# Optimization experiments

Measured on AMD Instinct MI355X. Metric: run time of the kernel, lower is better.

The kernel has to match this reference:

```python
import jax, jax.numpy as jnp
import numpy as np

K = 16  # neighbors per node (dgl.knn_graph k)


def _knn_indices(centers, k):
    # pairwise squared distances [N, N]
    sq = jnp.sum(centers * centers, axis=1)
    d2 = sq[:, None] + sq[None, :] - 2.0 * (centers @ centers.T)
    # k nearest (includes self at distance ~0), edges: neighbor(src) -> node(dst)
    _, idx = jax.lax.top_k(-d2, k)  # [N, k]
    return idx


def _graph_conv(h, idx, src_norm, dst_norm, W, b):
    # DGL GraphConv, norm='both': D_out^{-1/2} A D_in^{-1/2} H W + b
    hs = h * src_norm[:, None]          # scale by out-degree^{-1/2}
    agg = jnp.sum(hs[idx], axis=1)      # sum over k neighbors -> [N, F]
    agg = agg * dst_norm                # in-degree is exactly k for knn graph
    return agg @ W + b


def setup_inputs() -> dict:
    key = jax.random.key(0)
    ks = jax.random.split(key, 8)
    N, D, H = 20000, 128, 256
    s_in, s_h = 1.0 / np.sqrt(D), 1.0 / np.sqrt(H)
    return {
        "x": jax.random.normal(ks[0], (N, D), dtype=jnp.float32),
        "centers": jax.random.normal(ks[1], (N, 3), dtype=jnp.float32),
        "W0": jax.random.normal(ks[2], (D, H), dtype=jnp.float32) * s_in,
        "b0": jnp.zeros((H,), dtype=jnp.float32),
        "W1": jax.random.normal(ks[3], (H, H), dtype=jnp.float32) * s_h,
        "b1": jnp.zeros((H,), dtype=jnp.float32),
        "W2": jax.random.normal(ks[4], (H, H), dtype=jnp.float32) * s_h,
        "b2": jnp.zeros((H,), dtype=jnp.float32),
        "Wf": jax.random.normal(ks[5], (H, 1), dtype=jnp.float32) * s_h,
        "bf": jnp.zeros((1,), dtype=jnp.float32),
    }


def reference(x, centers, W0, b0, W1, b1, W2, b2, Wf, bf):
    N = x.shape[0]
    idx = _knn_indices(centers, K)  # [N, K] src nodes per dst node
    # out-degree of each node = number of times it appears as a neighbor
    out_deg = jnp.zeros((N,), dtype=x.dtype).at[idx.reshape(-1)].add(1.0)
    src_norm = jax.lax.rsqrt(jnp.maximum(out_deg, 1.0))
    dst_norm = 1.0 / jnp.sqrt(jnp.asarray(K, dtype=x.dtype))  # in-degree == K
    h = x
    for W, b in ((W0, b0), (W1, b1), (W2, b2)):
        h = jax.nn.relu(_graph_conv(h, idx, src_norm, dst_norm, W, b))
    logits = (h @ Wf + bf).squeeze(-1)  # [N]
    return jax.nn.sigmoid(logits)
```

## Files before the change

### kernel.cpp

```cpp
#include <hip/hip_runtime.h>
#include <math.h>

#define KNN 16
#define G 32
#define G3 32768
#define MRING 31
#define FLTMAX 3.402823466e+38f

typedef __attribute__((ext_vector_type(8))) short short8x;
typedef __attribute__((ext_vector_type(4))) float f32x4;

__device__ __forceinline__ unsigned short bf16rn(float x) {
  unsigned u = __float_as_uint(x);
  unsigned r = (u + 0x7FFFu + ((u >> 16) & 1u)) >> 16;
  return (unsigned short)r;
}
__device__ __forceinline__ float bf16tof(unsigned short h) {
  return __uint_as_float(((unsigned)h) << 16);
}

__device__ __forceinline__ unsigned fkey(float f) {
  unsigned u = __float_as_uint(f);
  return (u & 0x80000000u) ? ~u : (u | 0x80000000u);
}
__device__ __forceinline__ float funkey(unsigned u) {
  unsigned b = (u & 0x80000000u) ? (u & 0x7FFFFFFFu) : ~u;
  return __uint_as_float(b);
}

__device__ __forceinline__ void cell_of(float x, float y, float z, const float* P,
                                        int& cx, int& cy, int& cz) {
  cx = min(G - 1, max(0, (int)((x - P[0]) * P[3])));
  cy = min(G - 1, max(0, (int)((y - P[1]) * P[4])));
  cz = min(G - 1, max(0, (int)((z - P[2]) * P[5])));
}

__global__ void init_kernel(int* __restrict__ counts, int* __restrict__ cursor,
                            unsigned* __restrict__ bbox) {
  int t = blockIdx.x * blockDim.x + threadIdx.x;
  if (t < G3) counts[t] = 0;
  int u = t - G3;
  if (u >= 0 && u < G3) cursor[u] = 0;
  if (t == 0) {
    for (int k = 0; k < 3; ++k) { bbox[k] = 0xFFFFFFFFu; bbox[3 + k] = 0u; }
  }
}

__global__ void prep_kernel(const float* __restrict__ centers,
                            float4* __restrict__ cpack,
                            int* __restrict__ deg, unsigned* __restrict__ bbox, int n) {
  #pragma clang fp contract(off)
  int i = blockIdx.x * blockDim.x + threadIdx.x;
  if (i < n) {
    float x = centers[3 * i], y = centers[3 * i + 1], z = centers[3 * i + 2];
    float sq = (x * x + y * y) + z * z;
    cpack[i] = make_float4(x, y, z, sq);
    deg[i] = 0;
    atomicMin(&bbox[0], fkey(x));
    atomicMin(&bbox[1], fkey(y));
    atomicMin(&bbox[2], fkey(z));
    atomicMax(&bbox[3], fkey(x));
    atomicMax(&bbox[4], fkey(y));
    atomicMax(&bbox[5], fkey(z));
  }
}

__global__ void params_kernel(const unsigned* __restrict__ bbox, float* __restrict__ P) {
  if (threadIdx.x == 0 && blockIdx.x == 0) {
    float xmin = funkey(bbox[0]), ymin = funkey(bbox[1]), zmin = funkey(bbox[2]);
    float xmax = funkey(bbox[3]), ymax = funkey(bbox[4]), zmax = funkey(bbox[5]);
    float ex = fmaxf(xmax - xmin, 1e-9f);
    float ey = fmaxf(ymax - ymin, 1e-9f);
    float ez = fmaxf(zmax - zmin, 1e-9f);
    P[0] = xmin; P[1] = ymin; P[2] = zmin;
    P[3] = (float)G / ex; P[4] = (float)G / ey; P[5] = (float)G / ez;
    P[6] = ex / (float)G; P[7] = ey / (float)G; P[8] = ez / (float)G;
    P[9] = fminf(P[6], fminf(P[7], P[8]));
  }
}

__global__ void count_kernel(const float4* __restrict__ cpack, const float* __restrict__ P,
                             int* __restrict__ counts, int n) {
  int i = blockIdx.x * blockDim.x + threadIdx.x;
  if (i >= n) return;
  float4 c = cpack[i];
  int cx, cy, cz; cell_of(c.x, c.y, c.z, P, cx, cy, cz);
  atomicAdd(&counts[(cz * G + cy) * G + cx], 1);
}

__global__ __launch_bounds__(1024) void scan_kernel(const int* __restrict__ counts,
                                                    int* __restrict__ starts,
                                                    int2* __restrict__ cellinfo) {
  __shared__ int sh[1024];
  int t = threadIdx.x;
  int base = t * 32;
  int loc[32];
  int cnts[32];
  int s = 0;
  #pragma unroll
  for (int u = 0; u < 32; ++u) {
    cnts[u] = counts[base + u];
    loc[u] = s; s += cnts[u];
  }
  sh[t] = s;
  __syncthreads();
  for (int off = 1; off < 1024; off <<= 1) {
    int v = (t >= off) ? sh[t - off] : 0;
    __syncthreads();
    sh[t] += v;
    __syncthreads();
  }
  int pre = (t == 0) ? 0 : sh[t - 1];
  #pragma unroll
  for (int u = 0; u < 32; ++u) {
    int st = pre + loc[u];
    starts[base + u] = st;
    cellinfo[base + u] = make_int2(st, cnts[u]);
  }
}

__global__ void scatter_kernel(const float4* __restrict__ cpack, const float* __restrict__ P,
                               const int* __restrict__ starts, int* __restrict__ cursor,
                               int* __restrict__ sid, float4* __restrict__ spack, int n) {
  int i = blockIdx.x * blockDim.x + threadIdx.x;
  if (i >= n) return;
  float4 c = cpack[i];
  int cx, cy, cz; cell_of(c.x, c.y, c.z, P, cx, cy, cz);
  int cell = (cz * G + cy) * G + cx;
  int slot = starts[cell] + atomicAdd(&cursor[cell], 1);
  sid[slot] = i;
  spack[slot] = c;
}

__global__ __launch_bounds__(256) void query_kernel(
    const float4* __restrict__ spack, const int* __restrict__ sid,
    const int2* __restrict__ cellinfo, const float* __restrict__ P,
    int* __restrict__ knn_idx, int* __restrict__ deg, int n) {
  #pragma clang fp contract(off)
  __shared__ unsigned long long lsk[4][KNN][64];
  const int lane = threadIdx.x & 63;
  const int wv = threadIdx.x >> 6;
  const int g = blockIdx.x * 4 + wv;
  if (g >= n) return;
  const float4 q = spack[g];
  const int me = sid[g];
  const float xmin = P[0], ymin = P[1], zmin = P[2];
  const float wx = P[6], wy = P[7], wz = P[8], wmin = P[9];
  int cx, cy, cz; cell_of(q.x, q.y, q.z, P, cx, cy, cz);

  int cnt = 0;
  unsigned long long wkey = 0; int wslot = 0;
  unsigned long long minkey = ~0ull; int minslot = 0;

  for (int m = 1; m <= MRING; ++m) {
    if (m >= 2) {
      float b = (float)(m - 1) * wmin;
      float b2 = b * b * 0.999f;
      unsigned long long tk = ((unsigned long long)fkey(b2)) << 32;
      int c = 0;
      for (int t = 0; t < cnt; ++t) c += (lsk[wv][t][lane] < tk) ? 1 : 0;
      #pragma unroll
      for (int off = 1; off < 64; off <<= 1) c += __shfl_xor(c, off);
      if (c >= KNN) break;
    }
    float lw = (cnt == KNN) ? funkey((unsigned)(wkey >> 32)) : FLTMAX;
    #pragma unroll
    for (int off = 1; off < 64; off <<= 1) lw = fminf(lw, __shfl_xor(lw, off));

    const int ncells = (m == 1) ? 27 : (24 * m * m + 2);
    for (int cb = 0; cb < ncells; cb += 64) {
      int f = cb + lane;
      int ccnt = 0, cs0 = 0;
      if (f < ncells) {
        int dx, dy, dz;
        if (m == 1) {
          dz = f / 9 - 1; int rem = f % 9; dy = rem / 3 - 1; dx = rem % 3 - 1;
        } else {
          int side = 2 * m + 1;
          int S1 = side * side;
          if (f < 2 * S1) {
            dz = (f < S1) ? -m : m;
            int i2 = (f < S1) ? f : f - S1;
            dy = i2 / side - m; dx = i2 % side - m;
          } else {
            int r = f - 2 * S1;
            int layer = r / (8 * m);
            int t2 = r - layer * 8 * m;
            dz = layer - (m - 1);
            if (t2 < side) { dy = -m; dx = t2 - m; }
            else if (t2 < 2 * side) { dy = m; dx = (t2 - side) - m; }
            else { int u = t2 - 2 * side; dx = (u & 1) ? m : -m; dy = (u >> 1) - (m - 1); }
          }
        }
        int x = cx + dx, y = cy + dy, z = cz + dz;
        if (x >= 0 && x < G && y >= 0 && y < G && z >= 0 && z < G) {
          int cell = (z * G + y) * G + x;
          int2 ci = cellinfo[cell];
          if (ci.y > 0) {
            float lox = xmin + (float)x * wx;
            float loy = ymin + (float)y * wy;
            float loz = zmin + (float)z * wz;
            float ddx = fmaxf(fmaxf(lox - q.x, q.x - (lox + wx)), 0.f);
            float ddy = fmaxf(fmaxf(loy - q.y, q.y - (loy + wy)), 0.f);
            float ddz = fmaxf(fmaxf(loz - q.z, q.z - (loz + wz)), 0.f);
            float cd2 = ddx * ddx + ddy * ddy + ddz * ddz;
            if (!(cd2 * 0.999f > lw)) { ccnt = ci.y; cs0 = ci.x; }
          }
        }
      }
      int inc = ccnt;
      #pragma unroll
      for (int off = 1; off < 64; off <<= 1) {
        int t = __shfl_up(inc, off);
        if (lane >= off) inc += t;
      }
      int total = __shfl(inc, 63);
      if (total == 0) continue;
      unsigned seg = ((unsigned)(inc - ccnt) << 16) | (unsigned)cs0;
      const int tmax = total - 1;

      int fc = lane;
      int fcc = min(fc, tmax);
      int lo = 0;
      #pragma unroll
      for (int s = 32; s >= 1; s >>= 1) {
        int cand = lo + s;
        unsigned o = __shfl(seg, cand & 63);
        if (cand < 64 && (int)(o >> 16) <= fcc) lo = cand;
      }
      unsigned o2 = __shfl(seg, lo);
      int src = (int)(o2 & 0xFFFFu) + (fcc - (int)(o2 >> 16));
      float4 c4 = spack[src];
      int j = sid[src];
      const int nloop = (total + 63) >> 6;
      for (int it = 0; it < nloop; ++it) {
        int fn = fc + 64;
        int fnc = min(fn, tmax);
        int lo2 = 0;
        #pragma unroll
        for (int s = 32; s >= 1; s >>= 1) {
          int cand = lo2 + s;
          unsigned o = __shfl(seg, cand & 63);
          if (cand < 64 && (int)(o >> 16) <= fnc) lo2 = cand;
        }
        unsigned o3 = __shfl(seg, lo2);
        int srcn = (int)(o3 & 0xFFFFu) + (fnc - (int)(o3 >> 16));
        float4 c4n = spack[srcn];
        int jn = sid[srcn];
        if (fc < total) {
          float dot = fmaf(q.z, c4.z, fmaf(q.y, c4.y, q.x * c4.x));
          float d2 = (q.w + c4.w) - 2.0f * dot;
          unsigned long long key =
              (((unsigned long long)fkey(d2)) << 32) | (unsigned)j;
          if (cnt < KNN) {
            lsk[wv][cnt][lane] = key;
            if (key < minkey) { minkey = key; minslot = cnt; }
            ++cnt;
            if (cnt == KNN) {
              wkey = 0; wslot = 0;
              #pragma unroll
              for (int u = 0; u < KNN; ++u) {
                unsigned long long k2 = lsk[wv][u][lane];
                if (k2 > wkey) { wkey = k2; wslot = u; }
              }
            }
          } else if (key < wkey) {
            lsk[wv][wslot][lane] = key;
            if (key < minkey) { minkey = key; minslot = wslot; }
            wkey = 0;
            #pragma unroll
            for (int u = 0; u < KNN; ++u) {
              unsigned long long k2 = lsk[wv][u][lane];
              if (k2 > wkey) { wkey = k2; wslot = u; }
            }
          }
        }
        fc = fn; c4 = c4n; j = jn;
      }
    }
  }

  unsigned long long mykey = 0;
  for (int t = 0; t < KNN; ++t) {
    unsigned long long k = minkey; int src = lane;
    #pragma unroll
    for (int off = 1; off < 64; off <<= 1) {
      unsigned long long ok = __shfl_xor(k, off);
      int os = __shfl_xor(src, off);
      if (ok < k) { k = ok; src = os; }
    }
    if (lane == t) mykey = k;
    if (lane == src) {
      lsk[wv][minslot][lane] = ~0ull;
      minkey = ~0ull; minslot = 0;
      for (int u = 0; u < cnt; ++u) {
        unsigned long long kk = lsk[wv][u][lane];
        if (kk < minkey) { minkey = kk; minslot = u; }
      }
    }
  }
  if (lane < KNN) {
    int j = (int)(unsigned)(mykey & 0xFFFFFFFFull);
    knn_idx[me * KNN + lane] = j;
    atomicAdd(&deg[j], 1);
  }
}

__global__ void norm_kernel(const int* __restrict__ deg, float* __restrict__ srcn, int n) {
  int i = blockIdx.x * blockDim.x + threadIdx.x;
  if (i < n) {
    float d = (float)max(deg[i], 1);
    srcn[i] = 1.0f / sqrtf(d);
  }
}

__global__ void split_w_kernel(const float* __restrict__ W,
                               unsigned short* __restrict__ wbh,
                               unsigned short* __restrict__ wbl, int K) {
  int t = blockIdx.x * blockDim.x + threadIdx.x;
  int noct = (K >> 5) * 1024;
  if (t >= noct) return;
  int kblk = t >> 10;
  int g = (t >> 6) & 15;
  int l = t & 63;
  int n = ((g >> 2) << 6) + ((g & 3) << 4) + (l & 15);
  int kbase = (kblk << 5) + ((l >> 4) << 3);
  #pragma unroll
  for (int j = 0; j < 8; ++j) {
    float w = W[(kbase + j) * 256 + n];
    unsigned short hi = bf16rn(w);
    wbh[t * 8 + j] = hi;
    wbl[t * 8 + j] = bf16rn(w - bf16tof(hi));
  }
}

template <int F>
__global__ __launch_bounds__(256) void agg_kernel(const float* __restrict__ h,
                                                  const float* __restrict__ srcn,
                                                  const int* __restrict__ idx,
                                                  unsigned short* __restrict__ ah,
                                                  unsigned short* __restrict__ al,
                                                  int n) {
  const int lane = threadIdx.x & 63;
  const int wv = threadIdx.x >> 6;
  const int i = blockIdx.x * 4 + wv;
  if (i >= n) return;
  constexpr int V = F / 64;
  if constexpr (V == 4) {
    float4 acc = make_float4(0.f, 0.f, 0.f, 0.f);
    #pragma unroll
    for (int k = 0; k < KNN; ++k) {
      int s = idx[i * KNN + k];
      float sn = srcn[s];
      float4 hv = ((const float4*)(h + (size_t)s * F))[lane];
      acc.x = fmaf(sn, hv.x, acc.x);
      acc.y = fmaf(sn, hv.y, acc.y);
      acc.z = fmaf(sn, hv.z, acc.z);
      acc.w = fmaf(sn, hv.w, acc.w);
    }
    acc.x *= 0.25f; acc.y *= 0.25f; acc.z *= 0.25f; acc.w *= 0.25f;
    ushort4 hh, ll;
    hh.x = bf16rn(acc.x); ll.x = bf16rn(acc.x - bf16tof(hh.x));
    hh.y = bf16rn(acc.y); ll.y = bf16rn(acc.y - bf16tof(hh.y));
    hh.z = bf16rn(acc.z); ll.z = bf16rn(acc.z - bf16tof(hh.z));
    hh.w = bf16rn(acc.w); ll.w = bf16rn(acc.w - bf16tof(hh.w));
    ((ushort4*)(ah + (size_t)i * F))[lane] = hh;
    ((ushort4*)(al + (size_t)i * F))[lane] = ll;
  } else {
    float2 acc = make_float2(0.f, 0.f);
    #pragma unroll
    for (int k = 0; k < KNN; ++k) {
      int s = idx[i * KNN + k];
      float sn = srcn[s];
      float2 hv = ((const float2*)(h + (size_t)s * F))[lane];
      acc.x = fmaf(sn, hv.x, acc.x);
      acc.y = fmaf(sn, hv.y, acc.y);
    }
    acc.x *= 0.25f; acc.y *= 0.25f;
    ushort2 hh, ll;
    hh.x = bf16rn(acc.x); ll.x = bf16rn(acc.x - bf16tof(hh.x));
    hh.y = bf16rn(acc.y); ll.y = bf16rn(acc.y - bf16tof(hh.y));
    ((ushort2*)(ah + (size_t)i * F))[lane] = hh;
    ((ushort2*)(al + (size_t)i * F))[lane] = ll;
  }
}

__global__ __launch_bounds__(256) void gemm_mfma(
    const unsigned short* __restrict__ ah, const unsigned short* __restrict__ al,
    const unsigned short* __restrict__ wbh, const unsigned short* __restrict__ wbl,
    const float* __restrict__ bias, float* __restrict__ C, int M, int Kd) {
  __shared__ unsigned short sa_h[2][64][8];
  __shared__ unsigned short sa_l[2][64][8];
  __shared__ unsigned short sb_h[16][64][8];
  __shared__ unsigned short sb_l[16][64][8];
  const int tid = threadIdx.x;
  const int lane = tid & 63;
  const int w = tid >> 6;
  const int mt0 = blockIdx.x * 32;

  f32x4 acc[2][4];
  #pragma unroll
  for (int ms = 0; ms < 2; ++ms)
    #pragma unroll
    for (int ns = 0; ns < 4; ++ns) acc[ms][ns] = (f32x4){0.f, 0.f, 0.f, 0.f};

  const int nkb = Kd >> 5;
  for (int kit = 0; kit < nkb; ++kit) {
    const int k0 = kit << 5;
    if (tid < 128) {
      int msub = tid >> 6, l = tid & 63;
      int row = mt0 + (msub << 4) + (l & 15);
      int kk = k0 + ((l >> 4) << 3);
      if (row < M) {
        *(uint4*)&sa_h[msub][l][0] = *(const uint4*)(ah + (size_t)row * Kd + kk);
        *(uint4*)&sa_l[msub][l][0] = *(const uint4*)(al + (size_t)row * Kd + kk);
      } else {
        uint4 z = make_uint4(0, 0, 0, 0);
        *(uint4*)&sa_h[msub][l][0] = z;
        *(uint4*)&sa_l[msub][l][0] = z;
      }
    }
    #pragma unroll
    for (int o = tid; o < 1024; o += 256) {
      size_t off = ((size_t)kit * 1024 + o) * 8;
      *(uint4*)&sb_h[o >> 6][o & 63][0] = *(const uint4*)(wbh + off);
      *(uint4*)&sb_l[o >> 6][o & 63][0] = *(const uint4*)(wbl + off);
    }
    __syncthreads();
    short8x a_h0 = *(const short8x*)&sa_h[0][lane][0];
    short8x a_h1 = *(const short8x*)&sa_h[1][lane][0];
    short8x a_l0 = *(const short8x*)&sa_l[0][lane][0];
    short8x a_l1 = *(const short8x*)&sa_l[1][lane][0];
    #pragma unroll
    for (int ns = 0; ns < 4; ++ns) {
      short8x b_h = *(const short8x*)&sb_h[w * 4 + ns][lane][0];
      short8x b_l = *(const short8x*)&sb_l[w * 4 + ns][lane][0];
      acc[0][ns] = __builtin_amdgcn_mfma_f32_16x16x32_bf16(a_h0, b_h, acc[0][ns], 0, 0, 0);
      acc[0][ns] = __builtin_amdgcn_mfma_f32_16x16x32_bf16(a_h0, b_l, acc[0][ns], 0, 0, 0);
      acc[0][ns] = __builtin_amdgcn_mfma_f32_16x16x32_bf16(a_l0, b_h, acc[0][ns], 0, 0, 0);
      acc[1][ns] = __builtin_amdgcn_mfma_f32_16x16x32_bf16(a_h1, b_h, acc[1][ns], 0, 0, 0);
      acc[1][ns] = __builtin_amdgcn_mfma_f32_16x16x32_bf16(a_h1, b_l, acc[1][ns], 0, 0, 0);
      acc[1][ns] = __builtin_amdgcn_mfma_f32_16x16x32_bf16(a_l1, b_h, acc[1][ns], 0, 0, 0);
    }
    __syncthreads();
  }

  const int col = lane & 15;
  const int rq = lane >> 4;
  #pragma unroll
  for (int ms = 0; ms < 2; ++ms) {
    #pragma unroll
    for (int ns = 0; ns < 4; ++ns) {
      int nn = (w << 6) + (ns << 4) + col;
      float bi = bias[nn];
      #pragma unroll
      for (int r = 0; r < 4; ++r) {
        int row = mt0 + (ms << 4) + (rq << 2) + r;
        if (row < M) C[(size_t)row * 256 + nn] = fmaxf(acc[ms][ns][r] + bi, 0.f);
      }
    }
  }
}

__global__ __launch_bounds__(256) void final_kernel(const float* __restrict__ h,
                                                    const float* __restrict__ Wf,
                                                    const float* __restrict__ bf,
                                                    float* __restrict__ out, int n) {
  const int lane = threadIdx.x & 63;
  const int wv = threadIdx.x >> 6;
  const int i = blockIdx.x * 4 + wv;
  if (i >= n) return;
  float4 hv = *(const float4*)(h + (size_t)i * 256 + lane * 4);
  float4 wf = *(const float4*)(Wf + lane * 4);
  float p = hv.x * wf.x + hv.y * wf.y + hv.z * wf.z + hv.w * wf.w;
  #pragma unroll
  for (int off = 32; off > 0; off >>= 1) p += __shfl_down(p, off);
  if (lane == 0) out[i] = 1.0f / (1.0f + expf(-(p + bf[0])));
}

extern "C" void kernel_launch(void* const* d_in, const int* in_sizes, int n_in,
                              void* d_out, int out_size, void* d_ws, size_t ws_size,
                              hipStream_t stream) {
  const float* x = (const float*)d_in[0];
  const float* centers = (const float*)d_in[1];
  const float* W0 = (const float*)d_in[2];
  const float* b0 = (const float*)d_in[3];
  const float* W1 = (const float*)d_in[4];
  const float* b1 = (const float*)d_in[5];
  const float* W2 = (const float*)d_in[6];
  const float* b2 = (const float*)d_in[7];
  const float* Wf = (const float*)d_in[8];
  const float* bf = (const float*)d_in[9];
  float* out = (float*)d_out;

  const int N = in_sizes[1] / 3;

  char* p = (char*)d_ws;
  auto alloc = [&](size_t bytes) {
    void* r = (void*)p;
    p += (bytes + 255) & ~(size_t)255;
    return r;
  };
  float4* cpack = (float4*)alloc((size_t)N * 16);
  int* deg = (int*)alloc((size_t)N * 4);
  float* srcn = (float*)alloc((size_t)N * 4);
  int* idx = (int*)alloc((size_t)N * KNN * 4);
  unsigned short* ahb = (unsigned short*)alloc((size_t)N * 256 * 2);
  unsigned short* alb = (unsigned short*)alloc((size_t)N * 256 * 2);
  float* hA = (float*)alloc((size_t)N * 256 * 4);
  unsigned* bbox = (unsigned*)alloc(6 * 4);
  float* P = (float*)alloc(16 * 4);
  int* counts = (int*)alloc((size_t)G3 * 4);
  int* starts = (int*)alloc((size_t)G3 * 4);
  int* cursor = (int*)alloc((size_t)G3 * 4);
  int2* cellinfo = (int2*)alloc((size_t)G3 * 8);
  int* sid = (int*)alloc((size_t)N * 4);
  float4* spack = (float4*)alloc((size_t)N * 16);
  unsigned short* w0h = (unsigned short*)alloc(128 * 256 * 2);
  unsigned short* w0l = (unsigned short*)alloc(128 * 256 * 2);
  unsigned short* w1h = (unsigned short*)alloc(256 * 256 * 2);
  unsigned short* w1l = (unsigned short*)alloc(256 * 256 * 2);
  unsigned short* w2h = (unsigned short*)alloc(256 * 256 * 2);
  unsigned short* w2l = (unsigned short*)alloc(256 * 256 * 2);
  (void)ws_size; (void)n_in; (void)out_size;

  const int nb = (N + 255) / 256;

  init_kernel<<<256, 256, 0, stream>>>(counts, cursor, bbox);
  prep_kernel<<<nb, 256, 0, stream>>>(centers, cpack, deg, bbox, N);
  split_w_kernel<<<(128 / 32) * 1024 / 256, 256, 0, stream>>>(W0, w0h, w0l, 128);
  split_w_kernel<<<(256 / 32) * 1024 / 256, 256, 0, stream>>>(W1, w1h, w1l, 256);
  split_w_kernel<<<(256 / 32) * 1024 / 256, 256, 0, stream>>>(W2, w2h, w2l, 256);
  params_kernel<<<1, 64, 0, stream>>>(bbox, P);
  count_kernel<<<nb, 256, 0, stream>>>(cpack, P, counts, N);
  scan_kernel<<<1, 1024, 0, stream>>>(counts, starts, cellinfo);
  scatter_kernel<<<nb, 256, 0, stream>>>(cpack, P, starts, cursor, sid, spack, N);
  query_kernel<<<(N + 3) / 4, 256, 0, stream>>>(spack, sid, cellinfo, P, idx,
                                                deg, N);
  norm_kernel<<<nb, 256, 0, stream>>>(deg, srcn, N);

  const int agrid = (N + 3) / 4;
  const int ggrid = (N + 31) / 32;

  agg_kernel<128><<<agrid, 256, 0, stream>>>(x, srcn, idx, ahb, alb, N);
  gemm_mfma<<<ggrid, 256, 0, stream>>>(ahb, alb, w0h, w0l, b0, hA, N, 128);

  agg_kernel<256><<<agrid, 256, 0, stream>>>(hA, srcn, idx, ahb, alb, N);
  gemm_mfma<<<ggrid, 256, 0, stream>>>(ahb, alb, w1h, w1l, b1, hA, N, 256);

  agg_kernel<256><<<agrid, 256, 0, stream>>>(hA, srcn, idx, ahb, alb, N);
  gemm_mfma<<<ggrid, 256, 0, stream>>>(ahb, alb, w2h, w2l, b2, hA, N, 256);

  final_kernel<<<agrid, 256, 0, stream>>>(hA, Wf, bf, out, N);
}
```

Before: 514.2 us.

## Process GNN layers in spatially sorted node order with XCD-aware block swizzle

```diff
diff --git a/kernel.cpp b/kernel.cpp
--- a/kernel.cpp
+++ b/kernel.cpp
@@ -121,7 +121,8 @@
 
 __global__ void scatter_kernel(const float4* __restrict__ cpack, const float* __restrict__ P,
                                const int* __restrict__ starts, int* __restrict__ cursor,
-                               int* __restrict__ sid, float4* __restrict__ spack, int n) {
+                               int* __restrict__ sid, int* __restrict__ inv,
+                               float4* __restrict__ spack, int n) {
   int i = blockIdx.x * blockDim.x + threadIdx.x;
   if (i >= n) return;
   float4 c = cpack[i];
@@ -129,21 +130,21 @@
   int cell = (cz * G + cy) * G + cx;
   int slot = starts[cell] + atomicAdd(&cursor[cell], 1);
   sid[slot] = i;
+  inv[i] = slot;
   spack[slot] = c;
 }
 
-__global__ __launch_bounds__(256) void query_kernel(
+__global__ __launch_bounds__(64) void query_kernel(
     const float4* __restrict__ spack, const int* __restrict__ sid,
-    const int2* __restrict__ cellinfo, const float* __restrict__ P,
-    int* __restrict__ knn_idx, int* __restrict__ deg, int n) {
+    const int* __restrict__ inv, const int2* __restrict__ cellinfo,
+    const float* __restrict__ P, int* __restrict__ knn_idx,
+    int* __restrict__ deg, int n) {
   #pragma clang fp contract(off)
-  __shared__ unsigned long long lsk[4][KNN][64];
-  const int lane = threadIdx.x & 63;
-  const int wv = threadIdx.x >> 6;
-  const int g = blockIdx.x * 4 + wv;
+  __shared__ unsigned long long lsk[KNN][64];
+  const int lane = threadIdx.x;
+  const int g = blockIdx.x;
   if (g >= n) return;
   const float4 q = spack[g];
-  const int me = sid[g];
   const float xmin = P[0], ymin = P[1], zmin = P[2];
   const float wx = P[6], wy = P[7], wz = P[8], wmin = P[9];
   int cx, cy, cz; cell_of(q.x, q.y, q.z, P, cx, cy, cz);
@@ -158,7 +159,7 @@
       float b2 = b * b * 0.999f;
       unsigned long long tk = ((unsigned long long)fkey(b2)) << 32;
       int c = 0;
-      for (int t = 0; t < cnt; ++t) c += (lsk[wv][t][lane] < tk) ? 1 : 0;
+      for (int t = 0; t < cnt; ++t) c += (lsk[t][lane] < tk) ? 1 : 0;
       #pragma unroll
       for (int off = 1; off < 64; off <<= 1) c += __shfl_xor(c, off);
       if (c >= KNN) break;
@@ -253,24 +254,24 @@
           unsigned long long key =
               (((unsigned long long)fkey(d2)) << 32) | (unsigned)j;
           if (cnt < KNN) {
-            lsk[wv][cnt][lane] = key;
+            lsk[cnt][lane] = key;
             if (key < minkey) { minkey = key; minslot = cnt; }
             ++cnt;
             if (cnt == KNN) {
               wkey = 0; wslot = 0;
               #pragma unroll
               for (int u = 0; u < KNN; ++u) {
-                unsigned long long k2 = lsk[wv][u][lane];
+                unsigned long long k2 = lsk[u][lane];
                 if (k2 > wkey) { wkey = k2; wslot = u; }
               }
             }
           } else if (key < wkey) {
-            lsk[wv][wslot][lane] = key;
+            lsk[wslot][lane] = key;
             if (key < minkey) { minkey = key; minslot = wslot; }
             wkey = 0;
             #pragma unroll
             for (int u = 0; u < KNN; ++u) {
-              unsigned long long k2 = lsk[wv][u][lane];
+              unsigned long long k2 = lsk[u][lane];
               if (k2 > wkey) { wkey = k2; wslot = u; }
             }
           }
@@ -291,18 +292,19 @@
     }
     if (lane == t) mykey = k;
     if (lane == src) {
-      lsk[wv][minslot][lane] = ~0ull;
+      lsk[minslot][lane] = ~0ull;
       minkey = ~0ull; minslot = 0;
       for (int u = 0; u < cnt; ++u) {
-        unsigned long long kk = lsk[wv][u][lane];
+        unsigned long long kk = lsk[u][lane];
         if (kk < minkey) { minkey = kk; minslot = u; }
       }
     }
   }
   if (lane < KNN) {
     int j = (int)(unsigned)(mykey & 0xFFFFFFFFull);
-    knn_idx[me * KNN + lane] = j;
-    atomicAdd(&deg[j], 1);
+    int js = inv[j];
+    knn_idx[g * KNN + lane] = js;
+    atomicAdd(&deg[js], 1);
   }
 }
 
@@ -334,8 +336,14 @@
   }
 }
 
+__device__ __forceinline__ int xcd_swizzle(int b, int grid8) {
+  int nch = grid8 >> 3;
+  return (b & 7) * nch + (b >> 3);
+}
+
 template <int F>
 __global__ __launch_bounds__(256) void agg_kernel(const float* __restrict__ h,
+                                                  const int* __restrict__ rmap,
                                                   const float* __restrict__ srcn,
                                                   const int* __restrict__ idx,
                                                   unsigned short* __restrict__ ah,
@@ -343,7 +351,8 @@
                                                   int n) {
   const int lane = threadIdx.x & 63;
   const int wv = threadIdx.x >> 6;
-  const int i = blockIdx.x * 4 + wv;
+  const int eb = xcd_swizzle(blockIdx.x, gridDim.x);
+  const int i = eb * 4 + wv;
   if (i >= n) return;
   constexpr int V = F / 64;
   if constexpr (V == 4) {
@@ -352,7 +361,8 @@
     for (int k = 0; k < KNN; ++k) {
       int s = idx[i * KNN + k];
       float sn = srcn[s];
-      float4 hv = ((const float4*)(h + (size_t)s * F))[lane];
+      int row = rmap ? rmap[s] : s;
+      float4 hv = ((const float4*)(h + (size_t)row * F))[lane];
       acc.x = fmaf(sn, hv.x, acc.x);
       acc.y = fmaf(sn, hv.y, acc.y);
       acc.z = fmaf(sn, hv.z, acc.z);
@@ -372,7 +382,8 @@
     for (int k = 0; k < KNN; ++k) {
       int s = idx[i * KNN + k];
       float sn = srcn[s];
-      float2 hv = ((const float2*)(h + (size_t)s * F))[lane];
+      int row = rmap ? rmap[s] : s;
+      float2 hv = ((const float2*)(h + (size_t)row * F))[lane];
       acc.x = fmaf(sn, hv.x, acc.x);
       acc.y = fmaf(sn, hv.y, acc.y);
     }
@@ -396,7 +407,9 @@
   const int tid = threadIdx.x;
   const int lane = tid & 63;
   const int w = tid >> 6;
-  const int mt0 = blockIdx.x * 32;
+  const int eb = xcd_swizzle(blockIdx.x, gridDim.x);
+  const int mt0 = eb * 32;
+  if (mt0 >= M) return;
 
   f32x4 acc[2][4];
   #pragma unroll
@@ -463,19 +476,21 @@
 }
 
 __global__ __launch_bounds__(256) void final_kernel(const float* __restrict__ h,
+                                                    const int* __restrict__ sid,
                                                     const float* __restrict__ Wf,
                                                     const float* __restrict__ bf,
                                                     float* __restrict__ out, int n) {
   const int lane = threadIdx.x & 63;
   const int wv = threadIdx.x >> 6;
-  const int i = blockIdx.x * 4 + wv;
+  const int eb = xcd_swizzle(blockIdx.x, gridDim.x);
+  const int i = eb * 4 + wv;
   if (i >= n) return;
   float4 hv = *(const float4*)(h + (size_t)i * 256 + lane * 4);
   float4 wf = *(const float4*)(Wf + lane * 4);
   float p = hv.x * wf.x + hv.y * wf.y + hv.z * wf.z + hv.w * wf.w;
   #pragma unroll
   for (int off = 32; off > 0; off >>= 1) p += __shfl_down(p, off);
-  if (lane == 0) out[i] = 1.0f / (1.0f + expf(-(p + bf[0])));
+  if (lane == 0) out[sid[i]] = 1.0f / (1.0f + expf(-(p + bf[0])));
 }
 
 extern "C" void kernel_launch(void* const* d_in, const int* in_sizes, int n_in,
@@ -515,6 +530,7 @@
   int* cursor = (int*)alloc((size_t)G3 * 4);
   int2* cellinfo = (int2*)alloc((size_t)G3 * 8);
   int* sid = (int*)alloc((size_t)N * 4);
+  int* inv = (int*)alloc((size_t)N * 4);
   float4* spack = (float4*)alloc((size_t)N * 16);
   unsigned short* w0h = (unsigned short*)alloc(128 * 256 * 2);
   unsigned short* w0l = (unsigned short*)alloc(128 * 256 * 2);
@@ -534,22 +550,21 @@
   params_kernel<<<1, 64, 0, stream>>>(bbox, P);
   count_kernel<<<nb, 256, 0, stream>>>(cpack, P, counts, N);
   scan_kernel<<<1, 1024, 0, stream>>>(counts, starts, cellinfo);
-  scatter_kernel<<<nb, 256, 0, stream>>>(cpack, P, starts, cursor, sid, spack, N);
-  query_kernel<<<(N + 3) / 4, 256, 0, stream>>>(spack, sid, cellinfo, P, idx,
-                                                deg, N);
+  scatter_kernel<<<nb, 256, 0, stream>>>(cpack, P, starts, cursor, sid, inv, spack, N);
+  query_kernel<<<N, 64, 0, stream>>>(spack, sid, inv, cellinfo, P, idx, deg, N);
   norm_kernel<<<nb, 256, 0, stream>>>(deg, srcn, N);
 
-  const int agrid = (N + 3) / 4;
-  const int ggrid = (N + 31) / 32;
-
-  agg_kernel<128><<<agrid, 256, 0, stream>>>(x, srcn, idx, ahb, alb, N);
+  const int agrid = ((N + 3) / 4 + 7) & ~7;
+  const int ggrid = (((N + 31) / 32) + 7) & ~7;
+
+  agg_kernel<128><<<agrid, 256, 0, stream>>>(x, sid, srcn, idx, ahb, alb, N);
   gemm_mfma<<<ggrid, 256, 0, stream>>>(ahb, alb, w0h, w0l, b0, hA, N, 128);
 
-  agg_kernel<256><<<agrid, 256, 0, stream>>>(hA, srcn, idx, ahb, alb, N);
+  agg_kernel<256><<<agrid, 256, 0, stream>>>(hA, nullptr, srcn, idx, ahb, alb, N);
   gemm_mfma<<<ggrid, 256, 0, stream>>>(ahb, alb, w1h, w1l, b1, hA, N, 256);
 
-  agg_kernel<256><<<agrid, 256, 0, stream>>>(hA, srcn, idx, ahb, alb, N);
+  agg_kernel<256><<<agrid, 256, 0, stream>>>(hA, nullptr, srcn, idx, ahb, alb, N);
   gemm_mfma<<<ggrid, 256, 0, stream>>>(ahb, alb, w2h, w2l, b2, hA, N, 256);
 
-  final_kernel<<<agrid, 256, 0, stream>>>(hA, Wf, bf, out, N);
-}
+  final_kernel<<<agrid, 256, 0, stream>>>(hA, sid, Wf, bf, out, N);
+}
```

Result: faster. 478.2 us (-7.0%).
